# Optimization experiments

Hardware: AMD Instinct MI355X
Metric: run time of the kernel (lower is better)

The kernel has to match this reference:

```python
import jax, jax.numpy as jnp
import numpy as np

N, E, B = 50000, 200000, 512
F0, H1, C2, EMB = 78, 10, 128, 128
SEQ, VOCAB, NF, KW = 1000, 26, 32, 8
LOUT = EMB - KW + 1  # 121


def setup_inputs() -> dict:
    key = jax.random.key(0)
    ks = jax.random.split(key, 20)
    nrm = lambda k, s: jax.random.normal(k, s, jnp.float32) * 0.05
    return dict(
        x=jax.random.normal(ks[0], (N, F0), jnp.float32),
        edge_index=jax.random.randint(ks[1], (2, E), 0, N),
        batch=(jnp.arange(N) * B) // N,  # balanced sorted node->graph ids, all segments non-empty
        target=jax.random.randint(ks[2], (B, SEQ), 0, VOCAB),
        W1=nrm(ks[3], (F0, H1 * F0)), a_src1=nrm(ks[4], (H1, F0)), a_dst1=nrm(ks[5], (H1, F0)), b1=jnp.zeros((H1 * F0,), jnp.float32),
        W2=nrm(ks[6], (H1 * F0, C2)), a_src2=nrm(ks[7], (1, C2)), a_dst2=nrm(ks[8], (1, C2)), b2=jnp.zeros((C2,), jnp.float32),
        fc_g1_w=nrm(ks[9], (C2, C2)), fc_g1_b=jnp.zeros((C2,), jnp.float32),
        emb=nrm(ks[10], (VOCAB, EMB)),
        conv_w=nrm(ks[11], (NF, SEQ, KW)), conv_b=jnp.zeros((NF,), jnp.float32),
        fc_xt_w=nrm(ks[12], (NF * LOUT, C2)), fc_xt_b=jnp.zeros((C2,), jnp.float32),
        fc1_w=nrm(ks[13], (2 * C2, 1024)), fc1_b=jnp.zeros((1024,), jnp.float32),
        fc2_w=nrm(ks[14], (1024, 256)), fc2_b=jnp.zeros((256,), jnp.float32),
        out_w=nrm(ks[15], (256, 1)), out_b=jnp.zeros((1,), jnp.float32),
    )


def gat_conv(x, src, dst, W, a_src, a_dst, b, heads):
    # PyG GATConv (eval mode): project, per-edge attn logits, segment softmax over dst, scatter-add
    n = x.shape[0]
    c = W.shape[1] // heads
    h = (x @ W).reshape(n, heads, c)                 # [N,H,C]
    al_s = (h * a_src).sum(-1)                       # [N,H]
    al_d = (h * a_dst).sum(-1)
    al = jax.nn.leaky_relu(al_s[src] + al_d[dst], 0.2)   # [E',H]
    amax = jax.ops.segment_max(al, dst, num_segments=n)
    ex = jnp.exp(al - amax[dst])
    den = jax.ops.segment_sum(ex, dst, num_segments=n)
    alpha = ex / (den[dst] + 1e-16)
    out = jax.ops.segment_sum(h[src] * alpha[:, :, None], dst, num_segments=n)  # [N,H,C]
    return out.reshape(n, heads * c) + b


def reference(x, edge_index, batch, target, W1, a_src1, a_dst1, b1, W2, a_src2, a_dst2, b2,
              fc_g1_w, fc_g1_b, emb, conv_w, conv_b, fc_xt_w, fc_xt_b,
              fc1_w, fc1_b, fc2_w, fc2_b, out_w, out_b):
    n = x.shape[0]
    loops = jnp.arange(n)
    src = jnp.concatenate([edge_index[0], loops])    # add self loops (PyG default)
    dst = jnp.concatenate([edge_index[1], loops])
    h = jax.nn.elu(gat_conv(x, src, dst, W1, a_src1, a_dst1, b1, H1))
    h = jax.nn.relu(gat_conv(h, src, dst, W2, a_src2, a_dst2, b2, 1))
    g = jax.ops.segment_max(h, batch, num_segments=B)            # global max pool per graph
    g = jax.nn.relu(g @ fc_g1_w + fc_g1_b)                       # [B,128]
    e = emb[target]                                              # [B,1000,128]
    conv = jax.lax.conv_general_dilated(e, conv_w, (1,), 'VALID',
                                        dimension_numbers=('NCH', 'OIH', 'NCH'))
    conv = jax.nn.relu(conv + conv_b[None, :, None])             # [B,32,121]
    xt = conv.reshape(B, NF * LOUT) @ fc_xt_w + fc_xt_b          # [B,128]
    xc = jnp.concatenate([g, xt], axis=1)                        # [B,256]
    xc = jax.nn.relu(xc @ fc1_w + fc1_b)
    xc = jax.nn.relu(xc @ fc2_w + fc2_b)
    return xc @ out_w + out_b                                    # [B,1]
```

## Files before the change

kernel.cpp:

```cpp
#include <hip/hip_runtime.h>
#include <hip/hip_bf16.h>

#define N_NODES 50000
#define N_EDGES 200000
#define BGRAPHS 512
#define F0c 78
#define H1c 10
#define HC1 780
#define HSTR 832
#define C2c 128
#define SEQc 1000
#define VOCABc 26
#define NFc 32
#define KWc 8
#define LOUTc 121
#define EMBc 128
#define KX 96
#define KXT 3872
#define MROWS 13312
#define KM 1024
#define W2TF_N (25*8*64*8)

typedef __attribute__((ext_vector_type(8))) short short8;
typedef __attribute__((ext_vector_type(4))) float f32x4;
typedef unsigned short u16;

static constexpr size_t alignup(size_t x) { return (x + 255) & ~size_t(255); }

static constexpr size_t A_HBUF = 0;
static constexpr size_t A_OUT1 = alignup(A_HBUF + size_t(N_NODES)*HSTR*2);
static constexpr size_t A_H2   = alignup(A_OUT1 + size_t(N_NODES)*HSTR*2);
static constexpr size_t A_W2T  = alignup(A_H2   + size_t(N_NODES)*C2c*4);
static constexpr size_t A_ALS1 = alignup(A_W2T  + size_t(C2c)*HSTR*2);
static constexpr size_t A_ALD1 = alignup(A_ALS1 + size_t(N_NODES)*H1c*4);
static constexpr size_t A_ALS2 = alignup(A_ALD1 + size_t(N_NODES)*H1c*4);
static constexpr size_t A_ALD2 = alignup(A_ALS2 + size_t(N_NODES)*4);
static constexpr size_t A_DEG  = alignup(A_ALD2 + size_t(N_NODES)*4);
static constexpr size_t A_OFFS = alignup(A_DEG  + size_t(N_NODES)*4);
static constexpr size_t A_CUR  = alignup(A_OFFS + size_t(N_NODES+1)*4);
static constexpr size_t A_CSRC = alignup(A_CUR  + size_t(N_NODES)*4);
static constexpr size_t A_XC   = alignup(A_CSRC + size_t(N_EDGES+N_NODES)*4);
static constexpr size_t A_Y1   = alignup(A_XC   + size_t(BGRAPHS)*256*4);
static constexpr size_t A_BOFF = alignup(A_Y1   + size_t(BGRAPHS)*1024*4);
static constexpr size_t A_BPAD = alignup(A_BOFF + size_t(BGRAPHS)*(VOCABc+1)*4);
static constexpr size_t A_WXT  = alignup(A_BPAD + size_t(HSTR)*4);
static constexpr size_t A_FXP  = alignup(A_WXT  + size_t(C2c)*KXT*2);
static constexpr size_t A_W1HP = alignup(A_FXP  + size_t(11)*BGRAPHS*C2c*4);
static constexpr size_t A_WSD  = alignup(A_W1HP + size_t(10)*80*96*2);
static constexpr size_t A_CWT  = alignup(A_WSD  + size_t(2)*H1c*F0c*4);
static constexpr size_t A_END  = alignup(A_CWT  + size_t(2)*256*KM*2);
static_assert(W2TF_N*2 <= size_t(C2c)*HSTR*2, "w2tf fits old slot");

static constexpr size_t A_HFIN = A_HBUF;
static constexpr size_t A_AMAT = alignup(A_HFIN + size_t(N_NODES)*C2c*4);
static constexpr size_t A_CVO  = alignup(A_AMAT + size_t(MROWS)*256*4);
static constexpr size_t A_M    = alignup(A_CVO  + size_t(BGRAPHS)*KXT*2);
static_assert(A_M + size_t(MROWS)*KM*2 <= size_t(N_NODES)*HSTR*2, "alias A overflow");
static constexpr size_t A_XPAD = A_OUT1;
static_assert(size_t(N_NODES)*KX*2 <= size_t(N_NODES)*HSTR*2, "alias B overflow");

__device__ __forceinline__ float bflo(unsigned u) { return __uint_as_float(u << 16); }
__device__ __forceinline__ float bfhi(unsigned u) { return __uint_as_float(u & 0xffff0000u); }
__device__ __forceinline__ u16 f2bf(float v) {
    __hip_bfloat16 b = __float2bfloat16(v);
    return *(u16*)&b;
}

#define GLOAD16(g, l) __builtin_amdgcn_global_load_lds( \
    (const __attribute__((address_space(1))) void*)(g), \
    (__attribute__((address_space(3))) void*)(l), 16, 0, 0)

__global__ void k_prep(const float* __restrict__ x, const float* __restrict__ W1,
                       const float* __restrict__ W2, const float* __restrict__ b1,
                       const float* __restrict__ fcxt_w, const float* __restrict__ conv_w,
                       const float* __restrict__ a_src1, const float* __restrict__ a_dst1,
                       __hip_bfloat16* __restrict__ xpad, __hip_bfloat16* __restrict__ w1hp,
                       u16* __restrict__ w2tf, float* __restrict__ bpad,
                       u16* __restrict__ wxt, float* __restrict__ wsd,
                       u16* __restrict__ cwt, int* __restrict__ deg) {
    int i = blockIdx.x*256 + threadIdx.x;
    const int R0 = N_NODES;
    const int R1 = R0 + N_NODES*KX;
    const int R2 = R1 + 10*80*96;
    const int R3 = R2 + W2TF_N;
    const int R4 = R3 + HSTR;
    const int R5 = R4 + C2c*KXT;
    const int R6 = R5 + 2*H1c*F0c;
    const int R7 = R6 + 256*KM;
    if (i < R0) {
        deg[i] = 1;
    } else if (i < R1) {
        int t = i - R0; int n = t / KX, c = t - n*KX;
        xpad[t] = __float2bfloat16(c < F0c ? x[(size_t)n*F0c + c] : 0.f);
    } else if (i < R2) {
        int t = i - R1; int hh = t / 7680, rem = t - hh*7680;
        int j = rem / 96, k = rem - j*96;
        w1hp[t] = __float2bfloat16((j < F0c && k < F0c) ? W1[(size_t)k*HC1 + hh*F0c + j] : 0.f);
    } else if (i < R3) {
        int t = i - R2; int frag = t >> 3, tt = t & 7;
        int m16 = frag & 15, quad = (frag >> 4) & 3, cbg = (frag >> 6) & 7, kstep = frag >> 9;
        int col = cbg*16 + m16;
        int k = kstep*32 + quad*8 + tt;
        int hh = k / 80, cc = k - hh*80;
        w2tf[t] = f2bf((cc < F0c) ? W2[(size_t)(hh*F0c + cc)*C2c + col] : 0.f);
    } else if (i < R4) {
        int p = i - R3; int hh = p / 80, cc = p - hh*80;
        bpad[p] = (hh < H1c && cc < F0c) ? b1[hh*F0c + cc] : 0.f;
    } else if (i < R5) {
        int t = i - R4; int frag = t >> 3, tt = t & 7;
        int lane = frag & 63, m16 = lane & 15, quad = lane >> 4;
        int ct = (frag >> 6) & 7, kt = frag >> 9;
        wxt[t] = f2bf(fcxt_w[(size_t)(kt*32 + quad*8 + tt)*C2c + (ct*16 + m16)]);
    } else if (i < R6) {
        int t = i - R5; int sd = t / (H1c*F0c), rem = t - sd*(H1c*F0c);
        int hh = rem / F0c, c = rem - hh*F0c;
        const float* a = sd ? a_dst1 : a_src1;
        float v = 0.f;
        for (int j = 0; j < F0c; j++) v += W1[(size_t)c*HC1 + hh*F0c + j] * a[hh*F0c + j];
        wsd[t] = v;
    } else if (i < R7) {
        int t = i - R6; int col = t >> 10, ii = t & (KM-1);
        int o = col >> 3, k = col & 7;
        float v = (ii < SEQc) ? conv_w[((size_t)o*SEQc + ii)*KWc + k] : 0.f;
        u16 h = f2bf(v);
        float hv = __uint_as_float((unsigned)h << 16);
        cwt[(size_t)col*KM + ii] = h;
        cwt[(size_t)256*KM + (size_t)col*KM + ii] = f2bf(v - hv);
    }
}
#define PREP_TOTAL (N_NODES + N_NODES*KX + 10*80*96 + W2TF_N + HSTR + C2c*KXT + 2*H1c*F0c + 256*KM)

__global__ void k_count(const int* __restrict__ ei, int* deg) {
    int i = blockIdx.x*256 + threadIdx.x;
    if (i < N_EDGES) atomicAdd(&deg[ei[N_EDGES + i]], 1);
}
__global__ void k_scan(const int* __restrict__ deg, int* __restrict__ off,
                       int* __restrict__ cur, int n) {
    __shared__ int wsum[16];
    __shared__ int s_carry;
    int tid = threadIdx.x, lane = tid & 63, wid = tid >> 6;
    if (tid == 0) s_carry = 0;
    __syncthreads();
    for (int base = 0; base < n; base += 1024) {
        int i = base + tid;
        int v0 = (i < n) ? deg[i] : 0;
        int v = v0;
        for (int d = 1; d < 64; d <<= 1) { int t = __shfl_up(v, d, 64); if (lane >= d) v += t; }
        if (lane == 63) wsum[wid] = v;
        __syncthreads();
        if (wid == 0) {
            int w = (lane < 16) ? wsum[lane] : 0;
            for (int d = 1; d < 16; d <<= 1) { int t = __shfl_up(w, d, 64); if (lane >= d) w += t; }
            if (lane < 16) wsum[lane] = w;
        }
        __syncthreads();
        int wprev = (wid > 0) ? wsum[wid-1] : 0;
        int carry = s_carry;
        if (i < n) { int o = carry + wprev + (v - v0); off[i] = o; cur[i] = o; }
        __syncthreads();
        if (tid == 0) s_carry = carry + wsum[15];
        __syncthreads();
    }
    if (tid == 0) off[n] = s_carry;
}
__global__ void k_fill(const int* __restrict__ ei, int* cur, int* __restrict__ csrc) {
    int i = blockIdx.x*256 + threadIdx.x;
    if (i < N_EDGES) {
        int s = ei[i], d = ei[N_EDGES + i];
        int p = atomicAdd(&cur[d], 1);
        csrc[p] = s;
    } else if (i < N_EDGES + N_NODES) {
        int n = i - N_EDGES;
        int p = atomicAdd(&cur[n], 1);
        csrc[p] = n;
    }
}
__global__ void k_sortcsr(const int* __restrict__ offs, int* __restrict__ csrc) {
    int n = blockIdx.x*256 + threadIdx.x;
    if (n >= N_NODES) return;
    int s = offs[n], e = offs[n+1];
    for (int i = s + 1; i < e; i++) {
        int v = csrc[i];
        int j = i - 1;
        while (j >= s && csrc[j] > v) { csrc[j+1] = csrc[j]; j--; }
        csrc[j+1] = v;
    }
}

__global__ void k_att1x(const float* __restrict__ x, const float* __restrict__ wsd,
                        float* __restrict__ als, float* __restrict__ ald) {
    int i = blockIdx.x*256 + threadIdx.x;
    if (i >= N_NODES*H1c) return;
    int n = i / H1c, hh = i - n*H1c;
    const float* xr = x + (size_t)n*F0c;
    const float* ws = wsd + hh*F0c;
    const float* wd = wsd + H1c*F0c + hh*F0c;
    float s1 = 0.f, s2 = 0.f;
    for (int c = 0; c < F0c; c++) { float v = xr[c]; s1 += v*ws[c]; s2 += v*wd[c]; }
    als[i] = s1; ald[i] = s2;
}

__global__ void k_agg1x(const unsigned* __restrict__ xpu, const float* __restrict__ als,
                        const float* __restrict__ ald, const int* __restrict__ offs,
                        const int* __restrict__ csrc, unsigned* __restrict__ xaggu) {
    constexpr int H = H1c;
    int dn = blockIdx.x, lane = threadIdx.x;
    int s = offs[dn], e = offs[dn+1], deg = e - s;
    __shared__ float wexp[64*H];
    __shared__ int   ssrc[64];
    __shared__ float ms[H], dinv_s[H];

    if (deg <= 64) {
        if (lane < deg) ssrc[lane] = csrc[s + lane];
        __syncthreads();
        for (int idx = lane; idx < deg*H; idx += 64) {
            int j = idx / H, hh = idx - j*H;
            float al = als[(size_t)ssrc[j]*H + hh] + ald[(size_t)dn*H + hh];
            wexp[idx] = (al >= 0.f) ? al : 0.2f*al;
        }
        __syncthreads();
        if (lane < H) {
            float m = -1e30f;
            for (int j = 0; j < deg; j++) m = fmaxf(m, wexp[j*H + lane]);
            float den = 0.f;
            for (int j = 0; j < deg; j++) den += __expf(wexp[j*H + lane] - m);
            ms[lane] = m; dinv_s[lane] = 1.f/(den + 1e-16f);
        }
        __syncthreads();
        for (int idx = lane; idx < deg*H; idx += 64) {
            int hh = idx % H;
            wexp[idx] = __expf(wexp[idx] - ms[hh]) * dinv_s[hh];
        }
        __syncthreads();
        if (lane < 40) {
            float accL[H], accH[H];
            #pragma unroll
            for (int hh = 0; hh < H; hh++) { accL[hh] = 0.f; accH[hh] = 0.f; }
            int j = 0;
            for (; j + 1 < deg; j += 2) {
                unsigned ua = xpu[(size_t)ssrc[j]*48 + lane];
                unsigned ub = xpu[(size_t)ssrc[j+1]*48 + lane];
                float a0 = bflo(ua), a1 = bfhi(ua), b0 = bflo(ub), b1 = bfhi(ub);
                #pragma unroll
                for (int hh = 0; hh < H; hh++) {
                    float wA = wexp[j*H + hh], wB = wexp[(j+1)*H + hh];
                    accL[hh] += wA*a0 + wB*b0;
                    accH[hh] += wA*a1 + wB*b1;
                }
            }
            if (j < deg) {
                unsigned ua = xpu[(size_t)ssrc[j]*48 + lane];
                float a0 = bflo(ua), a1 = bfhi(ua);
                #pragma unroll
                for (int hh = 0; hh < H; hh++) {
                    float wA = wexp[j*H + hh];
                    accL[hh] += wA*a0;
                    accH[hh] += wA*a1;
                }
            }
            #pragma unroll
            for (int hh = 0; hh < H; hh++) {
                unsigned p = (unsigned)f2bf(accL[hh]) | ((unsigned)f2bf(accH[hh]) << 16);
                xaggu[((size_t)dn*H + hh)*40 + lane] = p;
            }
        }
    } else {
        if (lane < H) {
            float adv = ald[(size_t)dn*H + lane];
            float m = -1e30f;
            for (int j = s; j < e; j++) {
                float al = als[(size_t)csrc[j]*H + lane] + adv;
                al = (al >= 0.f) ? al : 0.2f*al;
                m = fmaxf(m, al);
            }
            float den = 0.f;
            for (int j = s; j < e; j++) {
                float al = als[(size_t)csrc[j]*H + lane] + adv;
                al = (al >= 0.f) ? al : 0.2f*al;
                den += __expf(al - m);
            }
            ms[lane] = m; dinv_s[lane] = 1.f/(den + 1e-16f);
        }
        __syncthreads();
        if (lane < 40) {
            float accL[H], accH[H];
            #pragma unroll
            for (int hh = 0; hh < H; hh++) { accL[hh] = 0.f; accH[hh] = 0.f; }
            for (int j = s; j < e; j++) {
                int sj = csrc[j];
                unsigned ua = xpu[(size_t)sj*48 + lane];
                float a0 = bflo(ua), a1 = bfhi(ua);
                #pragma unroll
                for (int hh = 0; hh < H; hh++) {
                    float al = als[(size_t)sj*H + hh] + ald[(size_t)dn*H + hh];
                    al = (al >= 0.f) ? al : 0.2f*al;
                    float a = __expf(al - ms[hh]) * dinv_s[hh];
                    accL[hh] += a*a0;
                    accH[hh] += a*a1;
                }
            }
            #pragma unroll
            for (int hh = 0; hh < H; hh++) {
                unsigned p = (unsigned)f2bf(accL[hh]) | ((unsigned)f2bf(accH[hh]) << 16);
                xaggu[((size_t)dn*H + hh)*40 + lane] = p;
            }
        }
    }
}

__global__ void __launch_bounds__(512, 4)
k_fuse12(const short* __restrict__ xagg, const short* __restrict__ w1hp,
         const float* __restrict__ bpad, const short* __restrict__ w2tf,
         const float* __restrict__ a_src2, const float* __restrict__ a_dst2,
         float* __restrict__ Cout, float* __restrict__ als2, float* __restrict__ ald2) {
    __shared__ __attribute__((aligned(16))) short As[32*832];
    int tid = threadIdx.x;
    int wave = tid >> 6, lane = tid & 63;
    int m16 = lane & 15, quad = lane >> 4;
    int blockrow = blockIdx.x * 32;
    int rg = wave >> 2;

    {
        int hg = wave & 3;
        int rowc = min(blockrow + rg*16 + m16, N_NODES-1);
        for (int hh = hg; hh < H1c; hh += 4) {
            const short8* arow = (const short8*)(xagg + ((size_t)rowc*H1c + hh)*80);
            f32x4 acc1[5];
            #pragma unroll
            for (int ct = 0; ct < 5; ct++) acc1[ct] = (f32x4){0.f,0.f,0.f,0.f};
            #pragma unroll
            for (int kt = 0; kt < 3; kt++) {
                short8 af = arow[kt*4 + quad];
                #pragma unroll
                for (int ct = 0; ct < 5; ct++) {
                    const short8* brow = (const short8*)(w1hp + (size_t)(hh*80 + ct*16 + m16)*96);
                    acc1[ct] = __builtin_amdgcn_mfma_f32_16x16x32_bf16(af, brow[kt*4 + quad],
                                                                      acc1[ct], 0, 0, 0);
                }
            }
            #pragma unroll
            for (int ct = 0; ct < 5; ct++) {
                int col = hh*80 + ct*16 + m16;
                float bv = bpad[col];
                #pragma unroll
                for (int r = 0; r < 4; r++) {
                    int rl = rg*16 + quad*4 + r;
                    float v = acc1[ct][r] + bv;
                    v = (v > 0.f) ? v : (__expf(v) - 1.f);
                    *(u16*)((char*)As + rl*1664 + ((col*2) ^ ((rl & 7) << 4))) = f2bf(v);
                }
            }
        }
    }
    __syncthreads();

    int cg = wave & 3;
    f32x4 acc[2];
    acc[0] = (f32x4){0.f,0.f,0.f,0.f};
    acc[1] = (f32x4){0.f,0.f,0.f,0.f};
    int S = (m16 & 7) << 4;
    const char* asRow = (const char*)As + (size_t)(rg*16 + m16)*1664;
    const short8* bp = (const short8*)w2tf;
    #pragma unroll 5
    for (int kstep = 0; kstep < 25; kstep++) {
        short8 af = *(const short8*)(asRow + ((kstep*64 + quad*16) ^ S));
        short8 b0 = bp[(size_t)(kstep*8 + cg*2    )*64 + lane];
        short8 b1 = bp[(size_t)(kstep*8 + cg*2 + 1)*64 + lane];
        acc[0] = __builtin_amdgcn_mfma_f32_16x16x32_bf16(af, b0, acc[0], 0, 0, 0);
        acc[1] = __builtin_amdgcn_mfma_f32_16x16x32_bf16(af, b1, acc[1], 0, 0, 0);
    }

    float asv[2], adv[2];
    #pragma unroll
    for (int ct = 0; ct < 2; ct++) {
        asv[ct] = a_src2[cg*32 + ct*16 + m16];
        adv[ct] = a_dst2[cg*32 + ct*16 + m16];
    }
    #pragma unroll
    for (int ct = 0; ct < 2; ct++) {
        int col = cg*32 + ct*16 + m16;
        #pragma unroll
        for (int r = 0; r < 4; r++) {
            int orow = blockrow + rg*16 + quad*4 + r;
            if (orow < N_NODES) Cout[(size_t)orow*C2c + col] = acc[ct][r];
        }
    }

    __syncthreads();
    float* sred  = (float*)As;
    float* sredd = sred + 128;
    #pragma unroll
    for (int r = 0; r < 4; r++) {
        float s1 = 0.f, s2 = 0.f;
        #pragma unroll
        for (int ct = 0; ct < 2; ct++) { s1 += acc[ct][r]*asv[ct]; s2 += acc[ct][r]*adv[ct]; }
        #pragma unroll
        for (int d = 1; d < 16; d <<= 1) { s1 += __shfl_xor(s1, d, 64); s2 += __shfl_xor(s2, d, 64); }
        if (m16 == 0) {
            int rl = rg*16 + quad*4 + r;
            sred[rl*4 + cg] = s1;
            sredd[rl*4 + cg] = s2;
        }
    }
    __syncthreads();
    if (tid < 32) {
        int orow = blockrow + tid;
        if (orow < N_NODES) {
            als2[orow] = sred[tid*4+0] + sred[tid*4+1] + sred[tid*4+2] + sred[tid*4+3];
            ald2[orow] = sredd[tid*4+0] + sredd[tid*4+1] + sredd[tid*4+2] + sredd[tid*4+3];
        }
    }
}

__global__ void k_agg2(const float* __restrict__ h2, const float* __restrict__ als,
                       const float* __restrict__ ald, const int* __restrict__ offs,
                       const int* __restrict__ csrc, const float* __restrict__ b2,
                       float* __restrict__ out) {
    int dn = blockIdx.x, lane = threadIdx.x;
    int s = offs[dn], e = offs[dn+1], deg = e - s;
    __shared__ float wexp[128];
    __shared__ int ssrc[128];

    if (deg <= 128) {
        float adv = ald[dn];
        for (int j = lane; j < deg; j += 64) {
            int sj = csrc[s + j];
            ssrc[j] = sj;
            float al = als[sj] + adv;
            wexp[j] = (al >= 0.f) ? al : 0.2f*al;
        }
        __syncthreads();
        float m = -1e30f;
        for (int j = lane; j < deg; j += 64) m = fmaxf(m, wexp[j]);
        #pragma unroll
        for (int d = 32; d > 0; d >>= 1) m = fmaxf(m, __shfl_xor(m, d, 64));
        __syncthreads();
        float den = 0.f;
        for (int j = lane; j < deg; j += 64) {
            float ex = __expf(wexp[j] - m);
            wexp[j] = ex;
            den += ex;
        }
        #pragma unroll
        for (int d = 32; d > 0; d >>= 1) den += __shfl_xor(den, d, 64);
        float dinv = 1.f/(den + 1e-16f);
        __syncthreads();
        float2 acc = {0.f, 0.f};
        for (int j = 0; j < deg; j++) {
            float alpha = wexp[j] * dinv;
            float2 v = ((const float2*)(h2 + (size_t)ssrc[j]*C2c))[lane];
            acc.x += alpha*v.x; acc.y += alpha*v.y;
        }
        float2 o;
        o.x = fmaxf(acc.x + b2[2*lane], 0.f);
        o.y = fmaxf(acc.y + b2[2*lane+1], 0.f);
        ((float2*)(out + (size_t)dn*C2c))[lane] = o;
    } else {
        __shared__ float sm[2];
        if (lane == 0) {
            float adv = ald[dn];
            float m = -1e30f;
            for (int j = s; j < e; j++) {
                float al = als[csrc[j]] + adv;
                al = (al >= 0.f) ? al : 0.2f*al;
                m = fmaxf(m, al);
            }
            float den = 0.f;
            for (int j = s; j < e; j++) {
                float al = als[csrc[j]] + adv;
                al = (al >= 0.f) ? al : 0.2f*al;
                den += __expf(al - m);
            }
            sm[0] = m; sm[1] = 1.f/(den + 1e-16f);
        }
        __syncthreads();
        float m = sm[0], dinv = sm[1], adv = ald[dn];
        float2 acc = {0.f, 0.f};
        for (int j = s; j < e; j++) {
            int sj = csrc[j];
            float al = als[sj] + adv;
            al = (al >= 0.f) ? al : 0.2f*al;
            float alpha = __expf(al - m) * dinv;
            float2 v = ((const float2*)(h2 + (size_t)sj*C2c))[lane];
            acc.x += alpha*v.x; acc.y += alpha*v.y;
        }
        float2 o;
        o.x = fmaxf(acc.x + b2[2*lane], 0.f);
        o.y = fmaxf(acc.y + b2[2*lane+1], 0.f);
        ((float2*)(out + (size_t)dn*C2c))[lane] = o;
    }
}

__global__ void k_poolfcg(const float* __restrict__ hf, const int* __restrict__ batch,
                          const float* __restrict__ W, const float* __restrict__ bias,
                          float* __restrict__ xc) {
    int b = blockIdx.x, tid = threadIdx.x;
    __shared__ int se[2];
    __shared__ float gs[C2c];
    if (tid < 2) {
        int key = b + tid;
        int lo = 0, hi = N_NODES;
        while (lo < hi) { int mid = (lo+hi) >> 1; if (batch[mid] < key) lo = mid+1; else hi = mid; }
        se[tid] = lo;
    }
    __syncthreads();
    int s = se[0], e = se[1];
    float m = -1e30f;
    for (int n = s; n < e; n++) m = fmaxf(m, hf[(size_t)n*C2c + tid]);
    gs[tid] = m;
    __syncthreads();
    float acc = bias[tid];
    for (int k = 0; k < C2c; k++) acc += gs[k] * W[k*C2c + tid];
    xc[b*256 + tid] = fmaxf(acc, 0.f);
}

__global__ void k_buildM(const int* __restrict__ target, u16* __restrict__ Mm) {
    int b = blockIdx.x, tid = threadIdx.x;
    short8 z = (short8){0,0,0,0,0,0,0,0};
    short8* base = (short8*)(Mm + (size_t)b*VOCABc*KM);
    for (int i = tid; i < VOCABc*KM/8; i += 256) base[i] = z;
    __syncthreads();
    for (int i = tid; i < SEQc; i += 256) {
        int t = target[(size_t)b*SEQc + i];
        Mm[((size_t)b*VOCABc + t)*KM + i] = (u16)0x3F80;
    }
}

__global__ void __launch_bounds__(256, 1)
k_amat_mfma(const short* __restrict__ Mm, const short* __restrict__ cwt,
            float* __restrict__ A2) {
    __shared__ __attribute__((aligned(16))) short As[2][128*64];
    __shared__ __attribute__((aligned(16))) short Bh[2][128*64];
    __shared__ __attribute__((aligned(16))) short Bl[2][128*64];
    int tid = threadIdx.x;
    int wave = tid >> 6, lane = tid & 63;
    int m16 = lane & 15, quad = lane >> 4;
    int blockrow = blockIdx.x * 128;
    int colbase  = blockIdx.y * 128;

    size_t aoff[4], bo[4];
    #pragma unroll
    for (int i = 0; i < 4; i++) {
        int c = wave*256 + i*64 + lane;
        int row = c >> 3;
        int cb  = (c & 7) << 4;
        int srcb = cb ^ ((row & 7) << 4);
        aoff[i] = (size_t)(blockrow + row) * (KM*2) + srcb;
        bo[i]   = (size_t)(colbase  + row) * (KM*2) + srcb;
    }
    const char* hbase = (const char*)cwt;
    const char* lbase = (const char*)(cwt + (size_t)256*KM);

    f32x4 acc[2][8];
    #pragma unroll
    for (int wr = 0; wr < 2; wr++)
        #pragma unroll
        for (int ct = 0; ct < 8; ct++) acc[wr][ct] = (f32x4){0.f,0.f,0.f,0.f};

    #pragma unroll
    for (int i = 0; i < 4; i++) {
        GLOAD16((const char*)Mm + aoff[i], &As[0][(wave*256 + i*64)*8]);
        GLOAD16(hbase + bo[i],             &Bh[0][(wave*256 + i*64)*8]);
        GLOAD16(lbase + bo[i],             &Bl[0][(wave*256 + i*64)*8]);
    }
    __syncthreads();

    int cur = 0;
    int S = (m16 & 7) << 4;
    for (int s = 0; s < KM/64; s++) {
        if (s + 1 < KM/64) {
            size_t kb = (size_t)(s + 1) * 128;
            #pragma unroll
            for (int i = 0; i < 4; i++) {
                GLOAD16((const char*)Mm + aoff[i] + kb, &As[cur^1][(wave*256 + i*64)*8]);
                GLOAD16(hbase + bo[i] + kb,             &Bh[cur^1][(wave*256 + i*64)*8]);
                GLOAD16(lbase + bo[i] + kb,             &Bl[cur^1][(wave*256 + i*64)*8]);
            }
        }
        const char* asBase = (const char*)&As[cur][0];
        const char* bhBase = (const char*)&Bh[cur][0];
        const char* blBase = (const char*)&Bl[cur][0];
        #pragma unroll
        for (int kk = 0; kk < 2; kk++) {
            int kb2 = (kk*64 + quad*16) ^ S;
            short8 af[2];
            #pragma unroll
            for (int wr = 0; wr < 2; wr++) {
                int row = wave*32 + wr*16 + m16;
                af[wr] = *(const short8*)(asBase + row*128 + kb2);
            }
            #pragma unroll
            for (int ct = 0; ct < 8; ct++) {
                int col = ct*16 + m16;
                short8 bhv = *(const short8*)(bhBase + col*128 + kb2);
                short8 blv = *(const short8*)(blBase + col*128 + kb2);
                acc[0][ct] = __builtin_amdgcn_mfma_f32_16x16x32_bf16(af[0], bhv, acc[0][ct], 0, 0, 0);
                acc[1][ct] = __builtin_amdgcn_mfma_f32_16x16x32_bf16(af[1], bhv, acc[1][ct], 0, 0, 0);
                acc[0][ct] = __builtin_amdgcn_mfma_f32_16x16x32_bf16(af[0], blv, acc[0][ct], 0, 0, 0);
                acc[1][ct] = __builtin_amdgcn_mfma_f32_16x16x32_bf16(af[1], blv, acc[1][ct], 0, 0, 0);
            }
        }
        __syncthreads();
        cur ^= 1;
    }

    #pragma unroll
    for (int wr = 0; wr < 2; wr++) {
        int rowbase = blockrow + wave*32 + wr*16 + quad*4;
        #pragma unroll
        for (int ct = 0; ct < 8; ct++) {
            int col = colbase + ct*16 + m16;
            #pragma unroll
            for (int r = 0; r < 4; r++) {
                A2[(size_t)(rowbase + r)*256 + col] = acc[wr][ct][r];
            }
        }
    }
}

__global__ void __launch_bounds__(128, 4)
k_conv(const float* __restrict__ A2, const float* __restrict__ emb,
       const float* __restrict__ convb, u16* __restrict__ convout) {
    int b = blockIdx.x, og = blockIdx.y;
    int tid = threadIdx.x;
    __shared__ float embs[VOCABc*EMBc];
    __shared__ float arow[4*VOCABc*KWc];
    for (int i = tid; i < VOCABc*EMBc; i += 128) embs[i] = emb[i];
    for (int i = tid; i < 4*VOCABc*KWc; i += 128) {
        int o2 = i / (VOCABc*KWc);
        int rem = i - o2*(VOCABc*KWc);
        int t = rem >> 3, k = rem & 7;
        arow[i] = A2[((size_t)b*VOCABc + t)*256 + (og*4 + o2)*8 + k];
    }
    __syncthreads();
    if (tid < LOUTc) {
        float a0 = convb[og*4+0], a1 = convb[og*4+1], a2 = convb[og*4+2], a3 = convb[og*4+3];
        for (int t = 0; t < VOCABc; t++) {
            #pragma unroll
            for (int k = 0; k < KWc; k++) {
                float ev = embs[t*EMBc + tid + k];
                a0 += arow[0*(VOCABc*KWc) + t*KWc + k] * ev;
                a1 += arow[1*(VOCABc*KWc) + t*KWc + k] * ev;
                a2 += arow[2*(VOCABc*KWc) + t*KWc + k] * ev;
                a3 += arow[3*(VOCABc*KWc) + t*KWc + k] * ev;
            }
        }
        size_t base = (size_t)b*KXT + (og*4)*LOUTc + tid;
        convout[base            ] = f2bf(fmaxf(a0, 0.f));
        convout[base +   LOUTc  ] = f2bf(fmaxf(a1, 0.f));
        convout[base + 2*LOUTc  ] = f2bf(fmaxf(a2, 0.f));
        convout[base + 3*LOUTc  ] = f2bf(fmaxf(a3, 0.f));
    }
}
__global__ void k_fcxt_mfma(const short* __restrict__ cvo, const short* __restrict__ wxt,
                            float* __restrict__ fxp) {
    int wave = threadIdx.x >> 6, lane = threadIdx.x & 63;
    int m16 = lane & 15, quad = lane >> 4;
    int r0 = blockIdx.x*64 + wave*16;
    int kt0 = blockIdx.y*11;
    const short8* arow = (const short8*)(cvo + (size_t)(r0 + m16)*KXT);
    const short8* bp = (const short8*)wxt;
    f32x4 acc[8];
    #pragma unroll
    for (int ct = 0; ct < 8; ct++) acc[ct] = (f32x4){0.f,0.f,0.f,0.f};
    for (int kt = kt0; kt < kt0 + 11; kt++) {
        short8 af = arow[kt*4 + quad];
        #pragma unroll
        for (int ct = 0; ct < 8; ct++) {
            short8 bf = bp[(size_t)(kt*8 + ct)*64 + lane];
            acc[ct] = __builtin_amdgcn_mfma_f32_16x16x32_bf16(af, bf, acc[ct], 0, 0, 0);
        }
    }
    #pragma unroll
    for (int ct = 0; ct < 8; ct++) {
        int col = ct*16 + m16;
        #pragma unroll
        for (int r = 0; r < 4; r++) {
            int row = r0 + quad*4 + r;
            fxp[((size_t)blockIdx.y*BGRAPHS + row)*C2c + col] = acc[ct][r];
        }
    }
}

__global__ void k_fc1(const float* __restrict__ xc, const float* __restrict__ fxp,
                      const float* __restrict__ fcxt_b, const float* __restrict__ W,
                      const float* __restrict__ bias, float* __restrict__ y1) {
    int b = blockIdx.x, tid = threadIdx.x;
    __shared__ float xs[256];
    if (tid < 128) {
        xs[tid] = xc[b*256 + tid];
    } else {
        int col = tid - 128;
        float s = fcxt_b[col];
        #pragma unroll
        for (int q = 0; q < 11; q++) s += fxp[((size_t)q*BGRAPHS + b)*C2c + col];
        xs[tid] = s;
    }
    __syncthreads();
    float a0 = bias[tid], a1 = bias[tid+256], a2 = bias[tid+512], a3 = bias[tid+768];
    for (int k = 0; k < 256; k++) {
        float xk = xs[k];
        const float* wr = W + (size_t)k*1024;
        a0 += xk*wr[tid]; a1 += xk*wr[tid+256]; a2 += xk*wr[tid+512]; a3 += xk*wr[tid+768];
    }
    y1[(size_t)b*1024 + tid      ] = fmaxf(a0, 0.f);
    y1[(size_t)b*1024 + tid + 256] = fmaxf(a1, 0.f);
    y1[(size_t)b*1024 + tid + 512] = fmaxf(a2, 0.f);
    y1[(size_t)b*1024 + tid + 768] = fmaxf(a3, 0.f);
}
__global__ void k_fc2out(const float* __restrict__ y1, const float* __restrict__ W,
                         const float* __restrict__ bias, const float* __restrict__ ow,
                         const float* __restrict__ ob, float* __restrict__ out) {
    int b = blockIdx.x, tid = threadIdx.x;
    int lane = tid & 63, wid = tid >> 6;
    __shared__ float ys[1024];
    __shared__ float wsum[4];
    for (int i = tid; i < 1024; i += 256) ys[i] = y1[(size_t)b*1024 + i];
    __syncthreads();
    float acc = bias[tid];
    for (int k = 0; k < 1024; k++) acc += ys[k] * W[(size_t)k*256 + tid];
    float v = fmaxf(acc, 0.f) * ow[tid];
    #pragma unroll
    for (int d = 32; d > 0; d >>= 1) v += __shfl_xor(v, d, 64);
    if (lane == 0) wsum[wid] = v;
    __syncthreads();
    if (tid == 0) out[b] = wsum[0] + wsum[1] + wsum[2] + wsum[3] + ob[0];
}

extern "C" void kernel_launch(void* const* d_in, const int* in_sizes, int n_in,
                              void* d_out, int out_size, void* d_ws, size_t ws_size,
                              hipStream_t stream) {
    (void)in_sizes; (void)n_in; (void)out_size;
    if (ws_size < A_END) return;

    const float* x       = (const float*)d_in[0];
    const int*   ei      = (const int*)  d_in[1];
    const int*   batch   = (const int*)  d_in[2];
    const int*   target  = (const int*)  d_in[3];
    const float* W1      = (const float*)d_in[4];
    const float* a_src1  = (const float*)d_in[5];
    const float* a_dst1  = (const float*)d_in[6];
    const float* b1      = (const float*)d_in[7];
    const float* W2      = (const float*)d_in[8];
    const float* a_src2  = (const float*)d_in[9];
    const float* a_dst2  = (const float*)d_in[10];
    const float* b2      = (const float*)d_in[11];
    const float* fcg_w   = (const float*)d_in[12];
    const float* fcg_b   = (const float*)d_in[13];
    const float* emb     = (const float*)d_in[14];
    const float* conv_w  = (const float*)d_in[15];
    const float* conv_b  = (const float*)d_in[16];
    const float* fcxt_w  = (const float*)d_in[17];
    const float* fcxt_b  = (const float*)d_in[18];
    const float* fc1_w   = (const float*)d_in[19];
    const float* fc1_b   = (const float*)d_in[20];
    const float* fc2_w   = (const float*)d_in[21];
    const float* fc2_b   = (const float*)d_in[22];
    const float* out_w   = (const float*)d_in[23];
    const float* out_b   = (const float*)d_in[24];

    char* wsb = (char*)d_ws;
    u16*   xagg  = (u16*)  (wsb + A_HBUF);
    float* h2    = (float*)(wsb + A_H2);
    u16*   w2tf  = (u16*)  (wsb + A_W2T);
    float* als1  = (float*)(wsb + A_ALS1);
    float* ald1  = (float*)(wsb + A_ALD1);
    float* als2  = (float*)(wsb + A_ALS2);
    float* ald2  = (float*)(wsb + A_ALD2);
    int*   deg   = (int*)  (wsb + A_DEG);
    int*   offs  = (int*)  (wsb + A_OFFS);
    int*   cur   = (int*)  (wsb + A_CUR);
    int*   csrc  = (int*)  (wsb + A_CSRC);
    float* xc    = (float*)(wsb + A_XC);
    float* y1    = (float*)(wsb + A_Y1);
    float* bpad  = (float*)(wsb + A_BPAD);
    u16*   wxt   = (u16*)  (wsb + A_WXT);
    float* fxp   = (float*)(wsb + A_FXP);
    __hip_bfloat16* w1hp = (__hip_bfloat16*)(wsb + A_W1HP);
    float* wsd   = (float*)(wsb + A_WSD);
    u16*   cwt   = (u16*)  (wsb + A_CWT);
    float* hfin  = (float*)(wsb + A_HFIN);
    float* Amat2 = (float*)(wsb + A_AMAT);
    u16*   cvo   = (u16*)  (wsb + A_CVO);
    u16*   Mm    = (u16*)  (wsb + A_M);
    __hip_bfloat16* xpad = (__hip_bfloat16*)(wsb + A_XPAD);

    k_prep<<<(PREP_TOTAL+255)/256, 256, 0, stream>>>(x, W1, W2, b1, fcxt_w, conv_w,
                                                     a_src1, a_dst1,
                                                     xpad, w1hp, w2tf, bpad, wxt, wsd, cwt, deg);
    k_count  <<<(N_EDGES+255)/256, 256, 0, stream>>>(ei, deg);
    k_scan   <<<1, 1024, 0, stream>>>(deg, offs, cur, N_NODES);
    k_fill   <<<(N_EDGES+N_NODES+255)/256, 256, 0, stream>>>(ei, cur, csrc);
    k_sortcsr<<<(N_NODES+255)/256, 256, 0, stream>>>(offs, csrc);

    k_att1x<<<(N_NODES*H1c+255)/256, 256, 0, stream>>>(x, wsd, als1, ald1);
    k_agg1x<<<N_NODES, 64, 0, stream>>>((const unsigned*)xpad, als1, ald1, offs, csrc,
                                        (unsigned*)xagg);

    k_fuse12<<<(N_NODES+31)/32, 512, 0, stream>>>((const short*)xagg, (const short*)w1hp,
                                                  bpad, (const short*)w2tf,
                                                  a_src2, a_dst2, h2, als2, ald2);

    k_buildM<<<BGRAPHS, 256, 0, stream>>>(target, Mm);

    k_agg2<<<N_NODES, 64, 0, stream>>>(h2, als2, ald2, offs, csrc, b2, hfin);

    k_poolfcg<<<BGRAPHS, 128, 0, stream>>>(hfin, batch, fcg_w, fcg_b, xc);

    k_amat_mfma<<<dim3(MROWS/128, 2), 256, 0, stream>>>((const short*)Mm, (const short*)cwt,
                                                        Amat2);
    k_conv  <<<dim3(BGRAPHS, 8), 128, 0, stream>>>(Amat2, emb, conv_b, cvo);
    k_fcxt_mfma<<<dim3(BGRAPHS/64, 11), 256, 0, stream>>>((const short*)cvo, (const short*)wxt, fxp);

    k_fc1<<<BGRAPHS, 256, 0, stream>>>(xc, fxp, fcxt_b, fc1_w, fc1_b, y1);
    k_fc2out<<<BGRAPHS, 256, 0, stream>>>(y1, fc2_w, fc2_b, out_w, out_b, (float*)d_out);
}
```

Before: 542.3 us.

## Shrink fused GAT projection kernel to 16-row blocks and prefetch head fragments

Each block of the fused layer-1-projection/layer-2-GEMM kernel now covers 16 nodes with 4 waves instead of 32 nodes with 8 waves. The block's LDS tile is halved and the launch bounds change to raise occupancy. Each wave loads the A fragments for all of its heads up front, then runs an unrolled per-head MFMA routine. The intent is more resident blocks and better latency hiding. The cost is twice as many blocks, each re-reading the W1/W2 weight fragments, and uneven head work across waves (two waves do three heads, two do two).

```diff
diff --git a/kernel.cpp b/kernel.cpp
--- a/kernel.cpp
+++ b/kernel.cpp
@@ -308,58 +308,66 @@
     }
 }
 
-__global__ void __launch_bounds__(512, 4)
+__global__ void __launch_bounds__(256, 6)
 k_fuse12(const short* __restrict__ xagg, const short* __restrict__ w1hp,
          const float* __restrict__ bpad, const short* __restrict__ w2tf,
          const float* __restrict__ a_src2, const float* __restrict__ a_dst2,
          float* __restrict__ Cout, float* __restrict__ als2, float* __restrict__ ald2) {
-    __shared__ __attribute__((aligned(16))) short As[32*832];
+    __shared__ __attribute__((aligned(16))) short As[16*832];
     int tid = threadIdx.x;
     int wave = tid >> 6, lane = tid & 63;
     int m16 = lane & 15, quad = lane >> 4;
-    int blockrow = blockIdx.x * 32;
-    int rg = wave >> 2;
+    int blockrow = blockIdx.x * 16;
 
     {
-        int hg = wave & 3;
-        int rowc = min(blockrow + rg*16 + m16, N_NODES-1);
-        for (int hh = hg; hh < H1c; hh += 4) {
-            const short8* arow = (const short8*)(xagg + ((size_t)rowc*H1c + hh)*80);
-            f32x4 acc1[5];
-            #pragma unroll
-            for (int ct = 0; ct < 5; ct++) acc1[ct] = (f32x4){0.f,0.f,0.f,0.f};
-            #pragma unroll
-            for (int kt = 0; kt < 3; kt++) {
-                short8 af = arow[kt*4 + quad];
-                #pragma unroll
-                for (int ct = 0; ct < 5; ct++) {
-                    const short8* brow = (const short8*)(w1hp + (size_t)(hh*80 + ct*16 + m16)*96);
-                    acc1[ct] = __builtin_amdgcn_mfma_f32_16x16x32_bf16(af, brow[kt*4 + quad],
-                                                                      acc1[ct], 0, 0, 0);
-                }
-            }
-            #pragma unroll
-            for (int ct = 0; ct < 5; ct++) {
-                int col = hh*80 + ct*16 + m16;
-                float bv = bpad[col];
-                #pragma unroll
-                for (int r = 0; r < 4; r++) {
-                    int rl = rg*16 + quad*4 + r;
-                    float v = acc1[ct][r] + bv;
-                    v = (v > 0.f) ? v : (__expf(v) - 1.f);
-                    *(u16*)((char*)As + rl*1664 + ((col*2) ^ ((rl & 7) << 4))) = f2bf(v);
-                }
-            }
-        }
-    }
-    __syncthreads();
-
-    int cg = wave & 3;
+        int hg = wave;
+        int rowc = min(blockrow + m16, N_NODES-1);
+        const short8* xr = (const short8*)(xagg + (size_t)rowc*H1c*80);
+        short8 afA[3], afB[3], afC[3];
+        #pragma unroll
+        for (int kt = 0; kt < 3; kt++) {
+            afA[kt] = xr[hg*10 + kt*4 + quad];
+            afB[kt] = xr[(hg+4)*10 + kt*4 + quad];
+            afC[kt] = xr[(hg+8)*10 + kt*4 + quad];
+        }
+#define COMPUTE_HEAD(hh, af) { \
+        f32x4 acc1[5]; \
+        _Pragma("unroll") \
+        for (int ct = 0; ct < 5; ct++) acc1[ct] = (f32x4){0.f,0.f,0.f,0.f}; \
+        _Pragma("unroll") \
+        for (int kt = 0; kt < 3; kt++) { \
+            _Pragma("unroll") \
+            for (int ct = 0; ct < 5; ct++) { \
+                const short8* brow = (const short8*)(w1hp + (size_t)((hh)*80 + ct*16 + m16)*96); \
+                acc1[ct] = __builtin_amdgcn_mfma_f32_16x16x32_bf16(af[kt], brow[kt*4 + quad], \
+                                                                  acc1[ct], 0, 0, 0); \
+            } \
+        } \
+        _Pragma("unroll") \
+        for (int ct = 0; ct < 5; ct++) { \
+            int col = (hh)*80 + ct*16 + m16; \
+            float bv = bpad[col]; \
+            _Pragma("unroll") \
+            for (int r = 0; r < 4; r++) { \
+                int rl = quad*4 + r; \
+                float v = acc1[ct][r] + bv; \
+                v = (v > 0.f) ? v : (__expf(v) - 1.f); \
+                *(u16*)((char*)As + rl*1664 + ((col*2) ^ ((rl & 7) << 4))) = f2bf(v); \
+            } \
+        } }
+        COMPUTE_HEAD(hg, afA)
+        COMPUTE_HEAD(hg+4, afB)
+        if (hg < 2) COMPUTE_HEAD(hg+8, afC)
+#undef COMPUTE_HEAD
+    }
+    __syncthreads();
+
+    int cg = wave;
     f32x4 acc[2];
     acc[0] = (f32x4){0.f,0.f,0.f,0.f};
     acc[1] = (f32x4){0.f,0.f,0.f,0.f};
     int S = (m16 & 7) << 4;
-    const char* asRow = (const char*)As + (size_t)(rg*16 + m16)*1664;
+    const char* asRow = (const char*)As + (size_t)m16*1664;
     const short8* bp = (const short8*)w2tf;
     #pragma unroll 5
     for (int kstep = 0; kstep < 25; kstep++) {
@@ -381,14 +389,14 @@
         int col = cg*32 + ct*16 + m16;
         #pragma unroll
         for (int r = 0; r < 4; r++) {
-            int orow = blockrow + rg*16 + quad*4 + r;
+            int orow = blockrow + quad*4 + r;
             if (orow < N_NODES) Cout[(size_t)orow*C2c + col] = acc[ct][r];
         }
     }
 
     __syncthreads();
     float* sred  = (float*)As;
-    float* sredd = sred + 128;
+    float* sredd = sred + 64;
     #pragma unroll
     for (int r = 0; r < 4; r++) {
         float s1 = 0.f, s2 = 0.f;
@@ -397,13 +405,13 @@
         #pragma unroll
         for (int d = 1; d < 16; d <<= 1) { s1 += __shfl_xor(s1, d, 64); s2 += __shfl_xor(s2, d, 64); }
         if (m16 == 0) {
-            int rl = rg*16 + quad*4 + r;
+            int rl = quad*4 + r;
             sred[rl*4 + cg] = s1;
             sredd[rl*4 + cg] = s2;
         }
     }
     __syncthreads();
-    if (tid < 32) {
+    if (tid < 16) {
         int orow = blockrow + tid;
         if (orow < N_NODES) {
             als2[orow] = sred[tid*4+0] + sred[tid*4+1] + sred[tid*4+2] + sred[tid*4+3];
@@ -797,7 +805,7 @@
     k_agg1x<<<N_NODES, 64, 0, stream>>>((const unsigned*)xpad, als1, ald1, offs, csrc,
                                         (unsigned*)xagg);
 
-    k_fuse12<<<(N_NODES+31)/32, 512, 0, stream>>>((const short*)xagg, (const short*)w1hp,
+    k_fuse12<<<(N_NODES+15)/16, 256, 0, stream>>>((const short*)xagg, (const short*)w1hp,
                                                   bpad, (const short*)w2tf,
                                                   a_src2, a_dst2, h2, als2, ald2);
 
```

New measurement: 548.6 us. About the same (+1.1%).
